# Performance work log

Hardware: AMD Instinct MI355X
Metric: run time of the kernel (lower is better)

Reference implementation:

```python
import jax, jax.numpy as jnp
import numpy as np

LAMBDA = 0.01

def setup_inputs() -> dict:
    key = jax.random.key(0)
    x = jax.random.normal(key, (32, 16384, 64), dtype=jnp.float32)
    return {"x": x}

def reference(x):
    # x: (B, N, D)
    B, N, D = x.shape
    mean = jnp.mean(x, axis=1, keepdims=True)          # (B, 1, D)
    diffs = x - mean                                    # (B, N, D)
    # Fused covariance: sum of centered outer products == GEMM, no (B,N,D,D) blowup
    cov = jnp.einsum('bnd,bne->bde', diffs, diffs) / (N - 1)  # (B, D, D)
    cov = cov + LAMBDA * jnp.eye(D, dtype=x.dtype)
    # torch.unique on the flattened symmetric matrices == globally sorted set of the
    # B * D*(D+1)/2 distinct entries (duplicates only arise from symmetry, prob-1 for
    # continuous inputs). Extract upper triangle per batch, then global sort.
    iu, ju = jnp.triu_indices(D)
    tri = cov[:, iu, ju]                                # (B, d_out)
    d_out = D * (D + 1) // 2
    return jnp.sort(tri.reshape(-1)).reshape(B, d_out)
```

## Files before the change

kernel.cpp:

```cpp
#include <hip/hip_runtime.h>
#include <stdint.h>


#define BATCHES 32
#define NSAMP   16384
#define DIM     64
#define LAMBDA  0.01f
#define NTRI    2080
#define NOUT    (BATCHES * NTRI)

#define CHUNKS_PER_BATCH 32
#define SAMP_PER_BLOCK   (NSAMP / CHUNKS_PER_BATCH)
#define SAMP_PER_WAVE    (SAMP_PER_BLOCK / 4)
#define PARTIAL_STRIDE   2624

typedef __attribute__((ext_vector_type(4))) float f32x4;
typedef __attribute__((ext_vector_type(8))) short s16x8;

__device__ __forceinline__ uint32_t f32_to_bf16(float f) {
    uint32_t u = __builtin_bit_cast(uint32_t, f);
    return (u + 0x7FFFu + ((u >> 16) & 1u)) >> 16;
}

__device__ __forceinline__ uint32_t sort_key(float v) {
    uint32_t u = __builtin_bit_cast(uint32_t, v);
    return u ^ (uint32_t)(((int32_t)u >> 31) | 0x80000000u);
}

__constant__ const int c_tmi[10] = {0, 0, 0, 0, 1, 1, 1, 2, 2, 3};
__constant__ const int c_tni[10] = {0, 1, 2, 3, 1, 2, 3, 2, 3, 3};

struct CovLds {
    float red[2][64][41];
    float msum_red[4][64];
};

template <typename EpilogueFn>
__device__ __forceinline__ void cov_body(const float* __restrict__ x, CovLds& L,
                                         EpilogueFn epi) {
    const int tid  = threadIdx.x;
    const int wave = tid >> 6;
    const int lane = tid & 63;
    const int b     = blockIdx.x / CHUNKS_PER_BATCH;
    const int chunk = blockIdx.x % CHUNKS_PER_BATCH;
    const int n_start = chunk * SAMP_PER_BLOCK + wave * SAMP_PER_WAVE;

    const int l15  = lane & 15;
    const int quad = lane >> 4;

    const float* xw = x + ((size_t)b * NSAMP + n_start) * DIM
                        + quad * 8 * DIM + l15;

    f32x4 acc[10];
#pragma unroll
    for (int t = 0; t < 10; ++t) acc[t] = (f32x4){0.f, 0.f, 0.f, 0.f};
    float sum_t[4] = {0.f, 0.f, 0.f, 0.f};

    for (int kc = 0; kc < SAMP_PER_WAVE / 32; ++kc) {
        const float* xs = xw + kc * 32 * DIM;
        float v[8][4];
#pragma unroll
        for (int j = 0; j < 8; ++j)
#pragma unroll
            for (int t = 0; t < 4; ++t)
                v[j][t] = xs[j * DIM + t * 16];

#pragma unroll
        for (int j = 0; j < 8; ++j)
#pragma unroll
            for (int t = 0; t < 4; ++t) sum_t[t] += v[j][t];

        s16x8 frag[4];
#pragma unroll
        for (int t = 0; t < 4; ++t) {
            uint32_t pk0 = f32_to_bf16(v[0][t]) | (f32_to_bf16(v[1][t]) << 16);
            uint32_t pk1 = f32_to_bf16(v[2][t]) | (f32_to_bf16(v[3][t]) << 16);
            uint32_t pk2 = f32_to_bf16(v[4][t]) | (f32_to_bf16(v[5][t]) << 16);
            uint32_t pk3 = f32_to_bf16(v[6][t]) | (f32_to_bf16(v[7][t]) << 16);
            frag[t] = __builtin_bit_cast(s16x8, make_uint4(pk0, pk1, pk2, pk3));
        }

        acc[0] = __builtin_amdgcn_mfma_f32_16x16x32_bf16(frag[0], frag[0], acc[0], 0, 0, 0);
        acc[1] = __builtin_amdgcn_mfma_f32_16x16x32_bf16(frag[0], frag[1], acc[1], 0, 0, 0);
        acc[2] = __builtin_amdgcn_mfma_f32_16x16x32_bf16(frag[0], frag[2], acc[2], 0, 0, 0);
        acc[3] = __builtin_amdgcn_mfma_f32_16x16x32_bf16(frag[0], frag[3], acc[3], 0, 0, 0);
        acc[4] = __builtin_amdgcn_mfma_f32_16x16x32_bf16(frag[1], frag[1], acc[4], 0, 0, 0);
        acc[5] = __builtin_amdgcn_mfma_f32_16x16x32_bf16(frag[1], frag[2], acc[5], 0, 0, 0);
        acc[6] = __builtin_amdgcn_mfma_f32_16x16x32_bf16(frag[1], frag[3], acc[6], 0, 0, 0);
        acc[7] = __builtin_amdgcn_mfma_f32_16x16x32_bf16(frag[2], frag[2], acc[7], 0, 0, 0);
        acc[8] = __builtin_amdgcn_mfma_f32_16x16x32_bf16(frag[2], frag[3], acc[8], 0, 0, 0);
        acc[9] = __builtin_amdgcn_mfma_f32_16x16x32_bf16(frag[3], frag[3], acc[9], 0, 0, 0);
    }

#pragma unroll
    for (int t = 0; t < 4; ++t) {
        sum_t[t] += __shfl_xor(sum_t[t], 16, 64);
        sum_t[t] += __shfl_xor(sum_t[t], 32, 64);
    }
    if (lane < 16) {
#pragma unroll
        for (int t = 0; t < 4; ++t) L.msum_red[wave][t * 16 + lane] = sum_t[t];
    }

    __syncthreads();
    if (wave == 1 || wave == 3) {
        int slot = wave >> 1;
#pragma unroll
        for (int t = 0; t < 10; ++t)
#pragma unroll
            for (int r = 0; r < 4; ++r) L.red[slot][lane][t * 4 + r] = acc[t][r];
    }
    __syncthreads();
    if (wave == 0 || wave == 2) {
        int slot = wave >> 1;
#pragma unroll
        for (int t = 0; t < 10; ++t)
#pragma unroll
            for (int r = 0; r < 4; ++r) acc[t][r] += L.red[slot][lane][t * 4 + r];
    }
    __syncthreads();
    if (wave == 2) {
#pragma unroll
        for (int t = 0; t < 10; ++t)
#pragma unroll
            for (int r = 0; r < 4; ++r) L.red[0][lane][t * 4 + r] = acc[t][r];
    }
    __syncthreads();
    if (wave == 0) {
#pragma unroll
        for (int t = 0; t < 10; ++t)
#pragma unroll
            for (int r = 0; r < 4; ++r) acc[t][r] += L.red[0][lane][t * 4 + r];
        float msum_tot = L.msum_red[0][lane] + L.msum_red[1][lane] +
                         L.msum_red[2][lane] + L.msum_red[3][lane];
        epi(b, lane, quad, l15, acc, msum_tot);
    }
}

__global__ __launch_bounds__(256, 4) void cov_kernel_p(const float* __restrict__ x,
                                                       float* __restrict__ partials) {
    __shared__ CovLds L;
    float* Pb = partials + (size_t)blockIdx.x * PARTIAL_STRIDE;
    cov_body(x, L, [&](int b, int lane, int quad, int l15, f32x4* acc, float msum) {
#pragma unroll
        for (int t = 0; t < 10; ++t)
#pragma unroll
            for (int r = 0; r < 4; ++r)
                Pb[t * 256 + r * 64 + lane] = acc[t][r];
        Pb[2560 + lane] = msum;
    });
}

__global__ __launch_bounds__(256, 4) void cov_kernel_a(const float* __restrict__ x,
                                                       float* __restrict__ S,
                                                       float* __restrict__ Msum) {
    __shared__ CovLds L;
    cov_body(x, L, [&](int b, int lane, int quad, int l15, f32x4* acc, float msum) {
        float* Sb = S + b * DIM * DIM;
#pragma unroll
        for (int t = 0; t < 10; ++t) {
            int d0 = c_tmi[t] * 16 + quad * 4;
            int e  = c_tni[t] * 16 + l15;
#pragma unroll
            for (int r = 0; r < 4; ++r)
                atomicAdd(&Sb[(d0 + r) * DIM + e], acc[t][r]);
        }
        atomicAdd(&Msum[b * DIM + lane], msum);
    });
}

__global__ __launch_bounds__(256) void reduce_kernel(const float* __restrict__ partials,
                                                     float* __restrict__ tri,
                                                     uint32_t* __restrict__ hist) {
    __shared__ float msum[DIM];
    const int b = blockIdx.x, tid = threadIdx.x;
    const float* P0 = partials + (size_t)b * CHUNKS_PER_BATCH * PARTIAL_STRIDE;

    float acc10[10];
#pragma unroll
    for (int k = 0; k < 10; ++k) acc10[k] = 0.f;
    float ms = 0.f;
    for (int c = 0; c < CHUNKS_PER_BATCH; ++c) {
        const float* P = P0 + c * PARTIAL_STRIDE;
#pragma unroll
        for (int k = 0; k < 10; ++k) acc10[k] += P[tid + 256 * k];
        if (tid < DIM) ms += P[2560 + tid];
    }
    if (tid < DIM) msum[tid] = ms;
    __syncthreads();

    const int r = tid >> 6, lane = tid & 63, quad = lane >> 4, l15 = lane & 15;
#pragma unroll
    for (int k = 0; k < 10; ++k) {
        int row = c_tmi[k] * 16 + quad * 4 + r;
        int col = c_tni[k] * 16 + l15;
        if (row <= col) {
            float v = (acc10[k] - msum[row] * msum[col] * (1.0f / NSAMP)) * (1.0f / (NSAMP - 1));
            if (row == col) v += LAMBDA;
            int p = row * 64 - (row * (row + 1)) / 2 + col;
            tri[b * NTRI + p] = v;
            atomicAdd(&hist[sort_key(v) >> 16], 1u);
        }
    }
}

__global__ void finalize_kernel(const float* __restrict__ S,
                                const float* __restrict__ Msum,
                                float* __restrict__ tri,
                                uint32_t* __restrict__ hist) {
    int t = blockIdx.x * blockDim.x + threadIdx.x;
    int b = t >> 12, de = t & 4095, d = de >> 6, e = de & 63;
    if (d > e) return;
    float ssum = S[b * 4096 + d * 64 + e];
    float md = Msum[b * 64 + d], me = Msum[b * 64 + e];
    float v = (ssum - md * me * (1.0f / NSAMP)) * (1.0f / (NSAMP - 1));
    if (d == e) v += LAMBDA;
    int p = d * 64 - (d * (d + 1)) / 2 + e;
    tri[b * NTRI + p] = v;
    atomicAdd(&hist[sort_key(v) >> 16], 1u);
}

__global__ __launch_bounds__(256) void scanA_kernel(const uint32_t* __restrict__ hist,
                                                    uint32_t* __restrict__ blocksums) {
    __shared__ uint32_t s[256];
    int tid = threadIdx.x;
    s[tid] = hist[blockIdx.x * 256 + tid];
    __syncthreads();
    for (int off = 128; off > 0; off >>= 1) {
        if (tid < off) s[tid] += s[tid + off];
        __syncthreads();
    }
    if (tid == 0) blocksums[blockIdx.x] = s[0];
}

__global__ __launch_bounds__(256) void scanB_kernel(const uint32_t* __restrict__ hist,
                                                    const uint32_t* __restrict__ blocksums,
                                                    uint32_t* __restrict__ offsets,
                                                    uint2* __restrict__ wl_small,
                                                    uint2* __restrict__ wl_large,
                                                    uint32_t* __restrict__ counts) {
    __shared__ uint32_t bs[256];
    __shared__ uint32_t sc[256];
    int tid = threadIdx.x, bid = blockIdx.x;

    bs[tid] = blocksums[tid];
    __syncthreads();
    for (int off = 1; off < 256; off <<= 1) {
        uint32_t a = (tid >= off) ? bs[tid - off] : 0u;
        __syncthreads();
        bs[tid] += a;
        __syncthreads();
    }
    uint32_t base = (bid > 0) ? bs[bid - 1] : 0u;

    uint32_t v = hist[bid * 256 + tid];
    sc[tid] = v;
    __syncthreads();
    for (int off = 1; off < 256; off <<= 1) {
        uint32_t a = (tid >= off) ? sc[tid - off] : 0u;
        __syncthreads();
        sc[tid] += a;
        __syncthreads();
    }
    uint32_t excl = base + sc[tid] - v;
    offsets[bid * 256 + tid] = excl;
    if (v >= 2u) {
        if (v <= 64u) {
            uint32_t w = atomicAdd(&counts[0], 1u);
            wl_small[w] = make_uint2(excl, v);
        } else {
            uint32_t w = atomicAdd(&counts[1], 1u);
            wl_large[w] = make_uint2(excl, v);
        }
    }
}

__global__ void scatter_kernel(const float* __restrict__ tri,
                               uint32_t* __restrict__ offsets,
                               float* __restrict__ out) {
    int i = blockIdx.x * blockDim.x + threadIdx.x;
    if (i >= NOUT) return;
    float v = tri[i];
    uint32_t pos = atomicAdd(&offsets[sort_key(v) >> 16], 1u);
    out[pos] = v;
}

__global__ __launch_bounds__(256) void runsort_small_kernel(float* __restrict__ out,
                                                            const uint2* __restrict__ wl,
                                                            const uint32_t* __restrict__ counts) {
    uint32_t nw = counts[0];
    int wave = threadIdx.x >> 6, lane = threadIdx.x & 63;
    for (uint32_t r = blockIdx.x * 4 + wave; r < nw; r += gridDim.x * 4) {
        uint2 e = wl[r];
        uint32_t start = e.x, cnt = e.y;
        float v = (lane < (int)cnt) ? out[start + lane] : __builtin_inff();
#pragma unroll
        for (uint32_t k = 2; k <= 64; k <<= 1)
            for (uint32_t j = k >> 1; j > 0; j >>= 1) {
                float p = __shfl_xor(v, (int)j, 64);
                bool keepmin = (((lane & k) == 0u) == ((lane & j) == 0u));
                v = keepmin ? fminf(v, p) : fmaxf(v, p);
            }
        if (lane < (int)cnt) out[start + lane] = v;
    }
}

#define SORT_CAP 8192
__global__ __launch_bounds__(256) void runsort_large_kernel(float* __restrict__ out,
                                                            const uint2* __restrict__ wl,
                                                            const uint32_t* __restrict__ counts) {
    __shared__ float buf[SORT_CAP];
    uint32_t nw = counts[1];
    for (uint32_t w = blockIdx.x; w < nw; w += gridDim.x) {
        uint2 ent = wl[w];
        uint32_t start = ent.x, cnt = ent.y;
        if (cnt > SORT_CAP) continue;
        uint32_t m = 1;
        while (m < cnt) m <<= 1;
        for (uint32_t i = threadIdx.x; i < m; i += blockDim.x)
            buf[i] = (i < cnt) ? out[start + i] : __builtin_inff();
        __syncthreads();
        for (uint32_t k = 2; k <= m; k <<= 1) {
            for (uint32_t j = k >> 1; j > 0; j >>= 1) {
                for (uint32_t i = threadIdx.x; i < m; i += blockDim.x) {
                    uint32_t ixj = i ^ j;
                    if (ixj > i) {
                        float a = buf[i], c = buf[ixj];
                        bool up = ((i & k) == 0u);
                        if ((a > c) == up) { buf[i] = c; buf[ixj] = a; }
                    }
                }
                __syncthreads();
            }
        }
        for (uint32_t i = threadIdx.x; i < cnt; i += blockDim.x)
            out[start + i] = buf[i];
        __syncthreads();
    }
}

extern "C" void kernel_launch(void* const* d_in, const int* in_sizes, int n_in,
                              void* d_out, int out_size, void* d_ws, size_t ws_size,
                              hipStream_t stream) {
    const float* x = (const float*)d_in[0];
    float* out = (float*)d_out;
    char* ws = (char*)d_ws;

    const size_t NEED_P = 1066048 + (size_t)1024 * PARTIAL_STRIDE * 4;

    if (ws_size >= NEED_P) {
        uint32_t* hist      = (uint32_t*)(ws);
        uint32_t* counts    = (uint32_t*)(ws + 262144);
        uint32_t* offsets   = (uint32_t*)(ws + 262208);
        uint32_t* blocksums = (uint32_t*)(ws + 524352);
        float*    tri       = (float*)(ws + 525376);
        uint2*    wl_small  = (uint2*)(ws + 791616);
        uint2*    wl_large  = (uint2*)(ws + 1057856);
        float*    partials  = (float*)(ws + 1066048);

        hipMemsetAsync(d_ws, 0, 262208, stream);
        cov_kernel_p<<<BATCHES * CHUNKS_PER_BATCH, 256, 0, stream>>>(x, partials);
        reduce_kernel<<<BATCHES, 256, 0, stream>>>(partials, tri, hist);
        scanA_kernel<<<256, 256, 0, stream>>>(hist, blocksums);
        scanB_kernel<<<256, 256, 0, stream>>>(hist, blocksums, offsets, wl_small, wl_large, counts);
        scatter_kernel<<<260, 256, 0, stream>>>(tri, offsets, out);
        runsort_small_kernel<<<128, 256, 0, stream>>>(out, wl_small, counts);
        runsort_large_kernel<<<64, 256, 0, stream>>>(out, wl_large, counts);
    } else {
        float*    S         = (float*)(ws);
        float*    Msum      = (float*)(ws + 524288);
        uint32_t* hist      = (uint32_t*)(ws + 532480);
        uint32_t* counts    = (uint32_t*)(ws + 794624);
        uint32_t* offsets   = (uint32_t*)(ws + 794688);
        uint32_t* blocksums = (uint32_t*)(ws + 1056832);
        float*    tri       = (float*)(ws + 1057856);
        uint2*    wl_small  = (uint2*)(ws + 1324096);
        uint2*    wl_large  = (uint2*)(ws + 1590336);

        hipMemsetAsync(d_ws, 0, 794688, stream);
        cov_kernel_a<<<BATCHES * CHUNKS_PER_BATCH, 256, 0, stream>>>(x, S, Msum);
        finalize_kernel<<<(BATCHES * 4096) / 256, 256, 0, stream>>>(S, Msum, tri, hist);
        scanA_kernel<<<256, 256, 0, stream>>>(hist, blocksums);
        scanB_kernel<<<256, 256, 0, stream>>>(hist, blocksums, offsets, wl_small, wl_large, counts);
        scatter_kernel<<<260, 256, 0, stream>>>(tri, offsets, out);
        runsort_small_kernel<<<128, 256, 0, stream>>>(out, wl_small, counts);
        runsort_large_kernel<<<64, 256, 0, stream>>>(out, wl_large, counts);
    }
}
```

Baseline: 333.1 us.

## Use finer 18-bit histogram buckets and merge run-sort kernels into one launch

Widens the bucket sort key from 16 to 18 bits so runs in each bucket are shorter and most can be sorted by the cheap wave-level bitonic path. The scan is adapted to 1024 blocks, with each thread summing four block sums. The two run-sort kernels are merged into a single 1024-block launch, and the covariance kernel's occupancy hint drops from 4 to 3. In exchange, the histogram memset, scan and offset arrays become four times larger.

```diff
diff --git a/kernel.cpp b/kernel.cpp
--- a/kernel.cpp
+++ b/kernel.cpp
@@ -13,6 +13,11 @@
 #define SAMP_PER_BLOCK   (NSAMP / CHUNKS_PER_BATCH)
 #define SAMP_PER_WAVE    (SAMP_PER_BLOCK / 4)
 #define PARTIAL_STRIDE   2624
+
+#define KEY_SHIFT 14
+#define NBUCKET   (1 << 18)
+#define SMALL_MAX 64u
+#define SORT_CAP  8192
 
 typedef __attribute__((ext_vector_type(4))) float f32x4;
 typedef __attribute__((ext_vector_type(8))) short s16x8;
@@ -137,7 +142,7 @@
     }
 }
 
-__global__ __launch_bounds__(256, 4) void cov_kernel_p(const float* __restrict__ x,
+__global__ __launch_bounds__(256, 3) void cov_kernel_p(const float* __restrict__ x,
                                                        float* __restrict__ partials) {
     __shared__ CovLds L;
     float* Pb = partials + (size_t)blockIdx.x * PARTIAL_STRIDE;
@@ -151,7 +156,7 @@
     });
 }
 
-__global__ __launch_bounds__(256, 4) void cov_kernel_a(const float* __restrict__ x,
+__global__ __launch_bounds__(256, 3) void cov_kernel_a(const float* __restrict__ x,
                                                        float* __restrict__ S,
                                                        float* __restrict__ Msum) {
     __shared__ CovLds L;
@@ -199,7 +204,7 @@
             if (row == col) v += LAMBDA;
             int p = row * 64 - (row * (row + 1)) / 2 + col;
             tri[b * NTRI + p] = v;
-            atomicAdd(&hist[sort_key(v) >> 16], 1u);
+            atomicAdd(&hist[sort_key(v) >> KEY_SHIFT], 1u);
         }
     }
 }
@@ -217,7 +222,7 @@
     if (d == e) v += LAMBDA;
     int p = d * 64 - (d * (d + 1)) / 2 + e;
     tri[b * NTRI + p] = v;
-    atomicAdd(&hist[sort_key(v) >> 16], 1u);
+    atomicAdd(&hist[sort_key(v) >> KEY_SHIFT], 1u);
 }
 
 __global__ __launch_bounds__(256) void scanA_kernel(const uint32_t* __restrict__ hist,
@@ -241,9 +246,13 @@
                                                     uint32_t* __restrict__ counts) {
     __shared__ uint32_t bs[256];
     __shared__ uint32_t sc[256];
+    __shared__ uint32_t base_sh;
     int tid = threadIdx.x, bid = blockIdx.x;
 
-    bs[tid] = blocksums[tid];
+    uint32_t b4[4]; uint32_t s4 = 0;
+#pragma unroll
+    for (int i = 0; i < 4; ++i) { b4[i] = blocksums[4 * tid + i]; s4 += b4[i]; }
+    bs[tid] = s4;
     __syncthreads();
     for (int off = 1; off < 256; off <<= 1) {
         uint32_t a = (tid >= off) ? bs[tid - off] : 0u;
@@ -251,7 +260,11 @@
         bs[tid] += a;
         __syncthreads();
     }
-    uint32_t base = (bid > 0) ? bs[bid - 1] : 0u;
+    if (tid == (bid >> 2)) {
+        uint32_t base = (tid > 0) ? bs[tid - 1] : 0u;
+        for (int i = 0; i < (bid & 3); ++i) base += b4[i];
+        base_sh = base;
+    }
 
     uint32_t v = hist[bid * 256 + tid];
     sc[tid] = v;
@@ -262,10 +275,10 @@
         sc[tid] += a;
         __syncthreads();
     }
-    uint32_t excl = base + sc[tid] - v;
+    uint32_t excl = base_sh + sc[tid] - v;
     offsets[bid * 256 + tid] = excl;
     if (v >= 2u) {
-        if (v <= 64u) {
+        if (v <= SMALL_MAX) {
             uint32_t w = atomicAdd(&counts[0], 1u);
             wl_small[w] = make_uint2(excl, v);
         } else {
@@ -281,38 +294,19 @@
     int i = blockIdx.x * blockDim.x + threadIdx.x;
     if (i >= NOUT) return;
     float v = tri[i];
-    uint32_t pos = atomicAdd(&offsets[sort_key(v) >> 16], 1u);
+    uint32_t pos = atomicAdd(&offsets[sort_key(v) >> KEY_SHIFT], 1u);
     out[pos] = v;
 }
 
-__global__ __launch_bounds__(256) void runsort_small_kernel(float* __restrict__ out,
-                                                            const uint2* __restrict__ wl,
-                                                            const uint32_t* __restrict__ counts) {
-    uint32_t nw = counts[0];
-    int wave = threadIdx.x >> 6, lane = threadIdx.x & 63;
-    for (uint32_t r = blockIdx.x * 4 + wave; r < nw; r += gridDim.x * 4) {
-        uint2 e = wl[r];
-        uint32_t start = e.x, cnt = e.y;
-        float v = (lane < (int)cnt) ? out[start + lane] : __builtin_inff();
-#pragma unroll
-        for (uint32_t k = 2; k <= 64; k <<= 1)
-            for (uint32_t j = k >> 1; j > 0; j >>= 1) {
-                float p = __shfl_xor(v, (int)j, 64);
-                bool keepmin = (((lane & k) == 0u) == ((lane & j) == 0u));
-                v = keepmin ? fminf(v, p) : fmaxf(v, p);
-            }
-        if (lane < (int)cnt) out[start + lane] = v;
-    }
-}
-
-#define SORT_CAP 8192
-__global__ __launch_bounds__(256) void runsort_large_kernel(float* __restrict__ out,
-                                                            const uint2* __restrict__ wl,
-                                                            const uint32_t* __restrict__ counts) {
+__global__ __launch_bounds__(256) void runsort_kernel(float* __restrict__ out,
+                                                      const uint2* __restrict__ wl_small,
+                                                      const uint2* __restrict__ wl_large,
+                                                      const uint32_t* __restrict__ counts) {
     __shared__ float buf[SORT_CAP];
-    uint32_t nw = counts[1];
-    for (uint32_t w = blockIdx.x; w < nw; w += gridDim.x) {
-        uint2 ent = wl[w];
+
+    uint32_t nl = counts[1];
+    for (uint32_t w = blockIdx.x; w < nl; w += gridDim.x) {
+        uint2 ent = wl_large[w];
         uint32_t start = ent.x, cnt = ent.y;
         if (cnt > SORT_CAP) continue;
         uint32_t m = 1;
@@ -337,6 +331,32 @@
             out[start + i] = buf[i];
         __syncthreads();
     }
+
+    uint32_t ns = counts[0];
+    int wave = threadIdx.x >> 6, lane = threadIdx.x & 63;
+    for (uint32_t r = blockIdx.x * 4 + wave; r < ns; r += gridDim.x * 4) {
+        uint2 e = wl_small[r];
+        uint32_t start = e.x, cnt = e.y;
+        float v = (lane < (int)cnt) ? out[start + lane] : __builtin_inff();
+#pragma unroll
+        for (uint32_t k = 2; k <= 64; k <<= 1)
+            for (uint32_t j = k >> 1; j > 0; j >>= 1) {
+                float p = __shfl_xor(v, (int)j, 64);
+                bool keepmin = (((lane & k) == 0u) == ((lane & j) == 0u));
+                v = keepmin ? fminf(v, p) : fmaxf(v, p);
+            }
+        if (lane < (int)cnt) out[start + lane] = v;
+    }
+}
+
+static void launch_tail(uint32_t* hist, uint32_t* blocksums, uint32_t* offsets,
+                        float* tri, uint2* wl_small, uint2* wl_large,
+                        uint32_t* counts, float* out, hipStream_t stream) {
+    scanA_kernel<<<NBUCKET / 256, 256, 0, stream>>>(hist, blocksums);
+    scanB_kernel<<<NBUCKET / 256, 256, 0, stream>>>(hist, blocksums, offsets,
+                                                    wl_small, wl_large, counts);
+    scatter_kernel<<<(NOUT + 255) / 256, 256, 0, stream>>>(tri, offsets, out);
+    runsort_kernel<<<1024, 256, 0, stream>>>(out, wl_small, wl_large, counts);
 }
 
 extern "C" void kernel_launch(void* const* d_in, const int* in_sizes, int n_in,
@@ -346,44 +366,36 @@
     float* out = (float*)d_out;
     char* ws = (char*)d_ws;
 
-    const size_t NEED_P = 1066048 + (size_t)1024 * PARTIAL_STRIDE * 4;
+    const size_t NEED_P = 2666560 + (size_t)1024 * PARTIAL_STRIDE * 4;
 
     if (ws_size >= NEED_P) {
         uint32_t* hist      = (uint32_t*)(ws);
-        uint32_t* counts    = (uint32_t*)(ws + 262144);
-        uint32_t* offsets   = (uint32_t*)(ws + 262208);
-        uint32_t* blocksums = (uint32_t*)(ws + 524352);
-        float*    tri       = (float*)(ws + 525376);
-        uint2*    wl_small  = (uint2*)(ws + 791616);
-        uint2*    wl_large  = (uint2*)(ws + 1057856);
-        float*    partials  = (float*)(ws + 1066048);
-
-        hipMemsetAsync(d_ws, 0, 262208, stream);
+        uint32_t* counts    = (uint32_t*)(ws + 1048576);
+        uint32_t* offsets   = (uint32_t*)(ws + 1048640);
+        uint32_t* blocksums = (uint32_t*)(ws + 2097216);
+        float*    tri       = (float*)(ws + 2101312);
+        uint2*    wl_small  = (uint2*)(ws + 2367552);
+        uint2*    wl_large  = (uint2*)(ws + 2633792);
+        float*    partials  = (float*)(ws + 2666560);
+
+        hipMemsetAsync(d_ws, 0, 1048640, stream);
         cov_kernel_p<<<BATCHES * CHUNKS_PER_BATCH, 256, 0, stream>>>(x, partials);
         reduce_kernel<<<BATCHES, 256, 0, stream>>>(partials, tri, hist);
-        scanA_kernel<<<256, 256, 0, stream>>>(hist, blocksums);
-        scanB_kernel<<<256, 256, 0, stream>>>(hist, blocksums, offsets, wl_small, wl_large, counts);
-        scatter_kernel<<<260, 256, 0, stream>>>(tri, offsets, out);
-        runsort_small_kernel<<<128, 256, 0, stream>>>(out, wl_small, counts);
-        runsort_large_kernel<<<64, 256, 0, stream>>>(out, wl_large, counts);
+        launch_tail(hist, blocksums, offsets, tri, wl_small, wl_large, counts, out, stream);
     } else {
         float*    S         = (float*)(ws);
         float*    Msum      = (float*)(ws + 524288);
         uint32_t* hist      = (uint32_t*)(ws + 532480);
-        uint32_t* counts    = (uint32_t*)(ws + 794624);
-        uint32_t* offsets   = (uint32_t*)(ws + 794688);
-        uint32_t* blocksums = (uint32_t*)(ws + 1056832);
-        float*    tri       = (float*)(ws + 1057856);
-        uint2*    wl_small  = (uint2*)(ws + 1324096);
-        uint2*    wl_large  = (uint2*)(ws + 1590336);
-
-        hipMemsetAsync(d_ws, 0, 794688, stream);
+        uint32_t* counts    = (uint32_t*)(ws + 1581056);
+        uint32_t* offsets   = (uint32_t*)(ws + 1581120);
+        uint32_t* blocksums = (uint32_t*)(ws + 2629696);
+        float*    tri       = (float*)(ws + 2633792);
+        uint2*    wl_small  = (uint2*)(ws + 2900032);
+        uint2*    wl_large  = (uint2*)(ws + 3166272);
+
+        hipMemsetAsync(d_ws, 0, 1581120, stream);
         cov_kernel_a<<<BATCHES * CHUNKS_PER_BATCH, 256, 0, stream>>>(x, S, Msum);
         finalize_kernel<<<(BATCHES * 4096) / 256, 256, 0, stream>>>(S, Msum, tri, hist);
-        scanA_kernel<<<256, 256, 0, stream>>>(hist, blocksums);
-        scanB_kernel<<<256, 256, 0, stream>>>(hist, blocksums, offsets, wl_small, wl_large, counts);
-        scatter_kernel<<<260, 256, 0, stream>>>(tri, offsets, out);
-        runsort_small_kernel<<<128, 256, 0, stream>>>(out, wl_small, counts);
-        runsort_large_kernel<<<64, 256, 0, stream>>>(out, wl_large, counts);
-    }
-}
+        launch_tail(hist, blocksums, offsets, tri, wl_small, wl_large, counts, out, stream);
+    }
+}
```

After: 313.7 us. 1.06x faster.
